# Kernel optimization log

Measured on AMD Instinct MI355X. Metric: run time of the kernel, lower is better.

## Reference

```python
import jax, jax.numpy as jnp
import numpy as np


def _cdist(A, B):
    # Euclidean distance matrix via the norm trick: ||a-b||^2 = |a|^2 + |b|^2 - 2 a.b
    # A: (M, D), B: (N, D) -> (M, N). Avoids materializing (M, N, D).
    a2 = jnp.sum(A * A, axis=-1)[:, None]
    b2 = jnp.sum(B * B, axis=-1)[None, :]
    d2 = a2 + b2 - 2.0 * (A @ B.T)
    return jnp.sqrt(jnp.maximum(d2, 0.0))


def _multiquadric(x):
    return jnp.sqrt(x * x + 1.0)


def setup_inputs() -> dict:
    key = jax.random.key(0)
    k1, k2, k3 = jax.random.split(key, 3)
    M, N, D, K = 16384, 8192, 3, 64
    Xp = jax.random.normal(k1, (M, D), dtype=jnp.float32)
    X = jax.random.normal(k2, (N, D), dtype=jnp.float32)
    W = jax.random.normal(k3, (K, N), dtype=jnp.float32)  # solved weights self.M: (K, N)
    eps = jnp.ones((), dtype=jnp.float32)
    return {"Xp": Xp, "X": X, "W": W, "eps": eps}


def reference(Xp, X, W, eps):
    # dist: (M, N) pairwise distances, phi = kernel(eps * dist)
    dist = _cdist(Xp, X)
    phi = _multiquadric(eps * dist)
    # Solve.forward: matmul(W, phi^T)^T == phi @ W^T -> (M, K)
    return phi @ W.T
```

## Files before the change

### kernel.cpp

```cpp
#include <hip/hip_runtime.h>
#include <hip/hip_bf16.h>
#include <stdint.h>

#define M_ROWS 16384
#define N_PTS  8192
#define K_OUT  64
#define NSPLIT 8
#define SLICE  (N_PTS / NSPLIT)

typedef short bf16x8 __attribute__((ext_vector_type(8)));
typedef float f32x4  __attribute__((ext_vector_type(4)));

union ABFrag { bf16x8 v; uint32_t u[4]; };
union BFrag  { uint4 q; bf16x8 v; };

__device__ __forceinline__ uint32_t pack_bf16_rhu(float a, float b) {
    uint32_t ua = __builtin_bit_cast(uint32_t, a) + 0x8000u;
    uint32_t ub = __builtin_bit_cast(uint32_t, b) + 0x8000u;
    return __builtin_amdgcn_perm(ub, ua, 0x07060302u);
}
__device__ __forceinline__ uint32_t pack_bf16_rne(float a, float b) {
    uint32_t ua = __builtin_bit_cast(uint32_t, a);
    ua += 0x7FFFu + ((ua >> 16) & 1u);
    uint32_t ub = __builtin_bit_cast(uint32_t, b);
    ub += 0x7FFFu + ((ub >> 16) & 1u);
    return __builtin_amdgcn_perm(ub, ua, 0x07060302u);
}

__global__ __launch_bounds__(256) void rbf_prep(
    const float* __restrict__ Wf, const float* __restrict__ X,
    const float* __restrict__ epsp, float* __restrict__ out,
    uint4* __restrict__ Wt, float* __restrict__ Xx,
    float* __restrict__ Xy, float* __restrict__ Xz)
{
    const int bid = blockIdx.x, tid = threadIdx.x;
    if (bid < 256) {
        const int kt = tid >> 6, lane = tid & 63;
        const int l15 = lane & 15, g = lane >> 4;
        const int row = kt * 16 + l15;
        const int col = bid * 32 + g * 8;
        const float4* src = (const float4*)(Wf + row * N_PTS + col);
        const float4 w0 = src[0], w1 = src[1];
        uint4 p;
        p.x = pack_bf16_rne(w0.x, w0.y);
        p.y = pack_bf16_rne(w0.z, w0.w);
        p.z = pack_bf16_rne(w1.x, w1.y);
        p.w = pack_bf16_rne(w1.z, w1.w);
        Wt[(bid * 4 + kt) * 64 + lane] = p;
    } else if (bid < 512) {
        const int i = ((bid - 256) * 256 + tid) * 4;
        const float4 z = make_float4(0.f, 0.f, 0.f, 0.f);
        float4* o = (float4*)out + i;
        o[0] = z; o[1] = z; o[2] = z; o[3] = z;
    } else {
        const int n = ((bid - 512) * 256 + tid) * 4;
        const float e = *epsp;
        const float4* p = (const float4*)(X + 3 * n);
        const float4 p0 = p[0], p1 = p[1], p2 = p[2];
        *(float4*)(Xx + n) = make_float4(p0.x * e, p0.w * e, p1.z * e, p2.y * e);
        *(float4*)(Xy + n) = make_float4(p0.y * e, p1.x * e, p1.w * e, p2.z * e);
        *(float4*)(Xz + n) = make_float4(p0.z * e, p1.y * e, p2.x * e, p2.w * e);
    }
}

__global__ __launch_bounds__(256, 4) void rbf_main(
    const float* __restrict__ Xp, const uint4* __restrict__ Wt,
    const float* __restrict__ Xx, const float* __restrict__ Xy,
    const float* __restrict__ Xz, const float* __restrict__ epsp,
    float* __restrict__ out)
{
    __shared__ float sX[SLICE], sY[SLICE], sZ[SLICE];

    const int tid  = threadIdx.x;
    const int lane = tid & 63;
    const int wv   = tid >> 6;
    const int l15  = lane & 15;
    const int g    = lane >> 4;

    const int bid  = blockIdx.x;
    const int ns   = bid & (NSPLIT - 1);
    const int rg   = bid >> 3;
    const int nbase = ns * SLICE;

    {
        const int i = tid * 4;
        *(float4*)(sX + i) = *(const float4*)(Xx + nbase + i);
        *(float4*)(sY + i) = *(const float4*)(Xy + nbase + i);
        *(float4*)(sZ + i) = *(const float4*)(Xz + nbase + i);
    }

    const float eps = *epsp;
    const int rowbase = rg * 128 + wv * 16;
    const int r0 = rowbase + l15;
    const int r1 = r0 + 64;
    const float px0 = Xp[r0 * 3 + 0] * eps, py0 = Xp[r0 * 3 + 1] * eps, pz0 = Xp[r0 * 3 + 2] * eps;
    const float px1 = Xp[r1 * 3 + 0] * eps, py1 = Xp[r1 * 3 + 1] * eps, pz1 = Xp[r1 * 3 + 2] * eps;

    __syncthreads();

    f32x4 acc00 = {0.f,0.f,0.f,0.f}, acc01 = acc00, acc02 = acc00, acc03 = acc00;
    f32x4 acc10 = acc00, acc11 = acc00, acc12 = acc00, acc13 = acc00;

    const uint4* wbase = Wt + (ns * 32) * 256 + lane;

    for (int s = 0; s < SLICE / 32; ++s) {
        const uint4* wp = wbase + s * 256;
        BFrag b0, b1, b2, b3;
        b0.q = wp[0];
        b1.q = wp[64];
        b2.q = wp[128];
        b3.q = wp[192];

        const int ci = s * 32 + g * 8;
        const float4 x0 = *(const float4*)(sX + ci), x1 = *(const float4*)(sX + ci + 4);
        const float4 y0 = *(const float4*)(sY + ci), y1 = *(const float4*)(sY + ci + 4);
        const float4 z0 = *(const float4*)(sZ + ci), z1 = *(const float4*)(sZ + ci + 4);

        const float xs[8] = {x0.x, x0.y, x0.z, x0.w, x1.x, x1.y, x1.z, x1.w};
        const float ys[8] = {y0.x, y0.y, y0.z, y0.w, y1.x, y1.y, y1.z, y1.w};
        const float zs[8] = {z0.x, z0.y, z0.z, z0.w, z1.x, z1.y, z1.z, z1.w};

        float t0[8], t1[8];
        #pragma unroll
        for (int j = 0; j < 8; ++j) {
            float dx = px0 - xs[j], dy = py0 - ys[j], dz = pz0 - zs[j];
            float d = fmaf(dx, dx, 1.0f); d = fmaf(dy, dy, d); d = fmaf(dz, dz, d);
            t0[j] = __builtin_amdgcn_sqrtf(d);
            dx = px1 - xs[j]; dy = py1 - ys[j]; dz = pz1 - zs[j];
            d = fmaf(dx, dx, 1.0f); d = fmaf(dy, dy, d); d = fmaf(dz, dz, d);
            t1[j] = __builtin_amdgcn_sqrtf(d);
        }

        ABFrag a0, a1;
        #pragma unroll
        for (int j = 0; j < 4; ++j) {
            a0.u[j] = pack_bf16_rhu(t0[2 * j], t0[2 * j + 1]);
            a1.u[j] = pack_bf16_rhu(t1[2 * j], t1[2 * j + 1]);
        }

        acc00 = __builtin_amdgcn_mfma_f32_16x16x32_bf16(a0.v, b0.v, acc00, 0, 0, 0);
        acc01 = __builtin_amdgcn_mfma_f32_16x16x32_bf16(a0.v, b1.v, acc01, 0, 0, 0);
        acc02 = __builtin_amdgcn_mfma_f32_16x16x32_bf16(a0.v, b2.v, acc02, 0, 0, 0);
        acc03 = __builtin_amdgcn_mfma_f32_16x16x32_bf16(a0.v, b3.v, acc03, 0, 0, 0);
        acc10 = __builtin_amdgcn_mfma_f32_16x16x32_bf16(a1.v, b0.v, acc10, 0, 0, 0);
        acc11 = __builtin_amdgcn_mfma_f32_16x16x32_bf16(a1.v, b1.v, acc11, 0, 0, 0);
        acc12 = __builtin_amdgcn_mfma_f32_16x16x32_bf16(a1.v, b2.v, acc12, 0, 0, 0);
        acc13 = __builtin_amdgcn_mfma_f32_16x16x32_bf16(a1.v, b3.v, acc13, 0, 0, 0);
    }

    float* o0 = out + (rowbase + g * 4) * K_OUT + l15;
    float* o1 = o0 + 64 * K_OUT;
    #pragma unroll
    for (int reg = 0; reg < 4; ++reg) {
        atomicAdd(o0 + reg * K_OUT +  0, acc00[reg]);
        atomicAdd(o0 + reg * K_OUT + 16, acc01[reg]);
        atomicAdd(o0 + reg * K_OUT + 32, acc02[reg]);
        atomicAdd(o0 + reg * K_OUT + 48, acc03[reg]);
        atomicAdd(o1 + reg * K_OUT +  0, acc10[reg]);
        atomicAdd(o1 + reg * K_OUT + 16, acc11[reg]);
        atomicAdd(o1 + reg * K_OUT + 32, acc12[reg]);
        atomicAdd(o1 + reg * K_OUT + 48, acc13[reg]);
    }
}

extern "C" void kernel_launch(void* const* d_in, const int* in_sizes, int n_in,
                              void* d_out, int out_size, void* d_ws, size_t ws_size,
                              hipStream_t stream) {
    (void)in_sizes; (void)n_in; (void)out_size; (void)ws_size;
    const float* Xp  = (const float*)d_in[0];
    const float* X   = (const float*)d_in[1];
    const float* Wf  = (const float*)d_in[2];
    const float* eps = (const float*)d_in[3];
    float* out = (float*)d_out;

    uint4* Wt = (uint4*)d_ws;
    float* Xx = (float*)((char*)d_ws + (1u << 20));
    float* Xy = Xx + N_PTS;
    float* Xz = Xy + N_PTS;

    rbf_prep<<<dim3(520), dim3(256), 0, stream>>>(Wf, X, eps, out, Wt, Xx, Xy, Xz);
    rbf_main<<<dim3((M_ROWS / 128) * NSPLIT), dim3(256), 0, stream>>>(Xp, Wt, Xx, Xy, Xz, eps, out);
}
```

Measured before the change: 111.3 us.

## Compute squared distances with MFMA via the norm trick, transpose phi through LDS

Replaces the per-element VALU distance computation with a bf16 MFMA that evaluates |p|^2 + |x|^2 + 1 - 2p·x from packed augmented vectors prepared in the prep kernel. The MFMA output layout is transposed through a small padded LDS tile to form the A operand of the phi·W^T MFMA. Rows per block are halved (grid doubled) and the occupancy hint is raised. The aim is to cut VALU work per phi element. The cost is bf16 precision on the coordinates and norms, which can cancel badly in the distance expansion, plus extra LDS traffic.

```diff
diff --git a/kernel.cpp b/kernel.cpp
--- a/kernel.cpp
+++ b/kernel.cpp
@@ -7,12 +7,12 @@
 #define K_OUT  64
 #define NSPLIT 8
 #define SLICE  (N_PTS / NSPLIT)
+#define LSTR   40
 
 typedef short bf16x8 __attribute__((ext_vector_type(8)));
 typedef float f32x4  __attribute__((ext_vector_type(4)));
 
-union ABFrag { bf16x8 v; uint32_t u[4]; };
-union BFrag  { uint4 q; bf16x8 v; };
+union ABFrag { bf16x8 v; uint32_t u[4]; uint4 q; };
 
 __device__ __forceinline__ uint32_t pack_bf16_rhu(float a, float b) {
     uint32_t ua = __builtin_bit_cast(uint32_t, a) + 0x8000u;
@@ -30,8 +30,7 @@
 __global__ __launch_bounds__(256) void rbf_prep(
     const float* __restrict__ Wf, const float* __restrict__ X,
     const float* __restrict__ epsp, float* __restrict__ out,
-    uint4* __restrict__ Wt, float* __restrict__ Xx,
-    float* __restrict__ Xy, float* __restrict__ Xz)
+    uint4* __restrict__ Wt, uint4* __restrict__ Pf)
 {
     const int bid = blockIdx.x, tid = threadIdx.x;
     if (bid < 256) {
@@ -53,113 +52,117 @@
         float4* o = (float4*)out + i;
         o[0] = z; o[1] = z; o[2] = z; o[3] = z;
     } else {
-        const int n = ((bid - 512) * 256 + tid) * 4;
-        const float e = *epsp;
-        const float4* p = (const float4*)(X + 3 * n);
-        const float4 p0 = p[0], p1 = p[1], p2 = p[2];
-        *(float4*)(Xx + n) = make_float4(p0.x * e, p0.w * e, p1.z * e, p2.y * e);
-        *(float4*)(Xy + n) = make_float4(p0.y * e, p1.x * e, p1.w * e, p2.z * e);
-        *(float4*)(Xz + n) = make_float4(p0.z * e, p1.y * e, p2.x * e, p2.w * e);
+        const int idx = (bid - 512) * 256 + tid;
+        const int lane = idx & 63;
+        const int t = idx >> 6;
+        const int g = lane >> 4, i = lane & 15;
+        uint4 v = make_uint4(0u, 0u, 0u, 0u);
+        if (g == 0) {
+            const int pt = t * 16 + i;
+            const float e = *epsp;
+            const float x = X[3 * pt + 0] * e;
+            const float y = X[3 * pt + 1] * e;
+            const float z = X[3 * pt + 2] * e;
+            const float b = fmaf(x, x, fmaf(y, y, fmaf(z, z, 1.0f)));
+            v.x = pack_bf16_rne(x, y);
+            v.y = pack_bf16_rne(z, b);
+            v.z = pack_bf16_rne(1.0f, 0.0f);
+        }
+        Pf[idx] = v;
     }
 }
 
-__global__ __launch_bounds__(256, 4) void rbf_main(
+__global__ __launch_bounds__(256, 5) void rbf_main(
     const float* __restrict__ Xp, const uint4* __restrict__ Wt,
-    const float* __restrict__ Xx, const float* __restrict__ Xy,
-    const float* __restrict__ Xz, const float* __restrict__ epsp,
+    const uint4* __restrict__ Pf, const float* __restrict__ epsp,
     float* __restrict__ out)
 {
-    __shared__ float sX[SLICE], sY[SLICE], sZ[SLICE];
+    __shared__ __align__(16) short sPhi[4 * 16 * LSTR];
 
     const int tid  = threadIdx.x;
     const int lane = tid & 63;
     const int wv   = tid >> 6;
-    const int l15  = lane & 15;
+    const int m    = lane & 15;
     const int g    = lane >> 4;
 
-    const int bid  = blockIdx.x;
-    const int ns   = bid & (NSPLIT - 1);
-    const int rg   = bid >> 3;
+    const int bid   = blockIdx.x;
+    const int ns    = bid & (NSPLIT - 1);
+    const int rg    = bid >> 3;
     const int nbase = ns * SLICE;
+    const int rowbase = rg * 64 + wv * 16;
 
-    {
-        const int i = tid * 4;
-        *(float4*)(sX + i) = *(const float4*)(Xx + nbase + i);
-        *(float4*)(sY + i) = *(const float4*)(Xy + nbase + i);
-        *(float4*)(sZ + i) = *(const float4*)(Xz + nbase + i);
+    ABFrag b1;
+    b1.q = make_uint4(0u, 0u, 0u, 0u);
+    if (g == 0) {
+        const float e = *epsp;
+        const int r = rowbase + m;
+        const float px = Xp[3 * r + 0] * e;
+        const float py = Xp[3 * r + 1] * e;
+        const float pz = Xp[3 * r + 2] * e;
+        const float a = fmaf(px, px, fmaf(py, py, pz * pz));
+        b1.u[0] = pack_bf16_rne(-2.0f * px, -2.0f * py);
+        b1.u[1] = pack_bf16_rne(-2.0f * pz, 1.0f);
+        b1.u[2] = pack_bf16_rne(a, 0.0f);
     }
 
-    const float eps = *epsp;
-    const int rowbase = rg * 128 + wv * 16;
-    const int r0 = rowbase + l15;
-    const int r1 = r0 + 64;
-    const float px0 = Xp[r0 * 3 + 0] * eps, py0 = Xp[r0 * 3 + 1] * eps, pz0 = Xp[r0 * 3 + 2] * eps;
-    const float px1 = Xp[r1 * 3 + 0] * eps, py1 = Xp[r1 * 3 + 1] * eps, pz1 = Xp[r1 * 3 + 2] * eps;
+    f32x4 acc0 = {0.f, 0.f, 0.f, 0.f};
+    f32x4 acc1 = acc0, acc2 = acc0, acc3 = acc0;
 
-    __syncthreads();
+    const uint4* pA = Pf + (nbase >> 4) * 64 + lane;
+    const uint4* wb = Wt + ns * 32 * 256 + lane;
+    short* wrow = sPhi + (wv * 16 + m) * LSTR;
 
-    f32x4 acc00 = {0.f,0.f,0.f,0.f}, acc01 = acc00, acc02 = acc00, acc03 = acc00;
-    f32x4 acc10 = acc00, acc11 = acc00, acc12 = acc00, acc13 = acc00;
+    #pragma unroll 2
+    for (int s = 0; s < SLICE / 32; ++s) {
+        ABFrag a1a, a1b;
+        a1a.q = pA[s * 128];
+        a1b.q = pA[s * 128 + 64];
 
-    const uint4* wbase = Wt + (ns * 32) * 256 + lane;
+        const uint4* wp = wb + s * 256;
+        ABFrag w0, w1, w2, w3;
+        w0.q = wp[0];
+        w1.q = wp[64];
+        w2.q = wp[128];
+        w3.q = wp[192];
 
-    for (int s = 0; s < SLICE / 32; ++s) {
-        const uint4* wp = wbase + s * 256;
-        BFrag b0, b1, b2, b3;
-        b0.q = wp[0];
-        b1.q = wp[64];
-        b2.q = wp[128];
-        b3.q = wp[192];
+        const f32x4 zc = {0.f, 0.f, 0.f, 0.f};
+        f32x4 d1a = __builtin_amdgcn_mfma_f32_16x16x32_bf16(a1a.v, b1.v, zc, 0, 0, 0);
+        f32x4 d1b = __builtin_amdgcn_mfma_f32_16x16x32_bf16(a1b.v, b1.v, zc, 0, 0, 0);
 
-        const int ci = s * 32 + g * 8;
-        const float4 x0 = *(const float4*)(sX + ci), x1 = *(const float4*)(sX + ci + 4);
-        const float4 y0 = *(const float4*)(sY + ci), y1 = *(const float4*)(sY + ci + 4);
-        const float4 z0 = *(const float4*)(sZ + ci), z1 = *(const float4*)(sZ + ci + 4);
+        float t0 = __builtin_amdgcn_sqrtf(fmaxf(d1a[0], 0.f));
+        float t1 = __builtin_amdgcn_sqrtf(fmaxf(d1a[1], 0.f));
+        float t2 = __builtin_amdgcn_sqrtf(fmaxf(d1a[2], 0.f));
+        float t3 = __builtin_amdgcn_sqrtf(fmaxf(d1a[3], 0.f));
+        float t4 = __builtin_amdgcn_sqrtf(fmaxf(d1b[0], 0.f));
+        float t5 = __builtin_amdgcn_sqrtf(fmaxf(d1b[1], 0.f));
+        float t6 = __builtin_amdgcn_sqrtf(fmaxf(d1b[2], 0.f));
+        float t7 = __builtin_amdgcn_sqrtf(fmaxf(d1b[3], 0.f));
 
-        const float xs[8] = {x0.x, x0.y, x0.z, x0.w, x1.x, x1.y, x1.z, x1.w};
-        const float ys[8] = {y0.x, y0.y, y0.z, y0.w, y1.x, y1.y, y1.z, y1.w};
-        const float zs[8] = {z0.x, z0.y, z0.z, z0.w, z1.x, z1.y, z1.z, z1.w};
+        uint2 pa, pb;
+        pa.x = pack_bf16_rhu(t0, t1);
+        pa.y = pack_bf16_rhu(t2, t3);
+        pb.x = pack_bf16_rhu(t4, t5);
+        pb.y = pack_bf16_rhu(t6, t7);
 
-        float t0[8], t1[8];
-        #pragma unroll
-        for (int j = 0; j < 8; ++j) {
-            float dx = px0 - xs[j], dy = py0 - ys[j], dz = pz0 - zs[j];
-            float d = fmaf(dx, dx, 1.0f); d = fmaf(dy, dy, d); d = fmaf(dz, dz, d);
-            t0[j] = __builtin_amdgcn_sqrtf(d);
-            dx = px1 - xs[j]; dy = py1 - ys[j]; dz = pz1 - zs[j];
-            d = fmaf(dx, dx, 1.0f); d = fmaf(dy, dy, d); d = fmaf(dz, dz, d);
-            t1[j] = __builtin_amdgcn_sqrtf(d);
-        }
+        *(uint2*)(wrow + 4 * g)      = pa;
+        *(uint2*)(wrow + 16 + 4 * g) = pb;
 
-        ABFrag a0, a1;
-        #pragma unroll
-        for (int j = 0; j < 4; ++j) {
-            a0.u[j] = pack_bf16_rhu(t0[2 * j], t0[2 * j + 1]);
-            a1.u[j] = pack_bf16_rhu(t1[2 * j], t1[2 * j + 1]);
-        }
+        ABFrag a2;
+        a2.q = *(const uint4*)(wrow + 8 * g);
 
-        acc00 = __builtin_amdgcn_mfma_f32_16x16x32_bf16(a0.v, b0.v, acc00, 0, 0, 0);
-        acc01 = __builtin_amdgcn_mfma_f32_16x16x32_bf16(a0.v, b1.v, acc01, 0, 0, 0);
-        acc02 = __builtin_amdgcn_mfma_f32_16x16x32_bf16(a0.v, b2.v, acc02, 0, 0, 0);
-        acc03 = __builtin_amdgcn_mfma_f32_16x16x32_bf16(a0.v, b3.v, acc03, 0, 0, 0);
-        acc10 = __builtin_amdgcn_mfma_f32_16x16x32_bf16(a1.v, b0.v, acc10, 0, 0, 0);
-        acc11 = __builtin_amdgcn_mfma_f32_16x16x32_bf16(a1.v, b1.v, acc11, 0, 0, 0);
-        acc12 = __builtin_amdgcn_mfma_f32_16x16x32_bf16(a1.v, b2.v, acc12, 0, 0, 0);
-        acc13 = __builtin_amdgcn_mfma_f32_16x16x32_bf16(a1.v, b3.v, acc13, 0, 0, 0);
+        acc0 = __builtin_amdgcn_mfma_f32_16x16x32_bf16(a2.v, w0.v, acc0, 0, 0, 0);
+        acc1 = __builtin_amdgcn_mfma_f32_16x16x32_bf16(a2.v, w1.v, acc1, 0, 0, 0);
+        acc2 = __builtin_amdgcn_mfma_f32_16x16x32_bf16(a2.v, w2.v, acc2, 0, 0, 0);
+        acc3 = __builtin_amdgcn_mfma_f32_16x16x32_bf16(a2.v, w3.v, acc3, 0, 0, 0);
     }
 
-    float* o0 = out + (rowbase + g * 4) * K_OUT + l15;
-    float* o1 = o0 + 64 * K_OUT;
+    float* o = out + (rowbase + g * 4) * K_OUT + m;
     #pragma unroll
     for (int reg = 0; reg < 4; ++reg) {
-        atomicAdd(o0 + reg * K_OUT +  0, acc00[reg]);
-        atomicAdd(o0 + reg * K_OUT + 16, acc01[reg]);
-        atomicAdd(o0 + reg * K_OUT + 32, acc02[reg]);
-        atomicAdd(o0 + reg * K_OUT + 48, acc03[reg]);
-        atomicAdd(o1 + reg * K_OUT +  0, acc10[reg]);
-        atomicAdd(o1 + reg * K_OUT + 16, acc11[reg]);
-        atomicAdd(o1 + reg * K_OUT + 32, acc12[reg]);
-        atomicAdd(o1 + reg * K_OUT + 48, acc13[reg]);
+        atomicAdd(o + reg * K_OUT +  0, acc0[reg]);
+        atomicAdd(o + reg * K_OUT + 16, acc1[reg]);
+        atomicAdd(o + reg * K_OUT + 32, acc2[reg]);
+        atomicAdd(o + reg * K_OUT + 48, acc3[reg]);
     }
 }
 
@@ -174,10 +177,8 @@
     float* out = (float*)d_out;
 
     uint4* Wt = (uint4*)d_ws;
-    float* Xx = (float*)((char*)d_ws + (1u << 20));
-    float* Xy = Xx + N_PTS;
-    float* Xz = Xy + N_PTS;
+    uint4* Pf = (uint4*)((char*)d_ws + (1u << 20));
 
-    rbf_prep<<<dim3(520), dim3(256), 0, stream>>>(Wf, X, eps, out, Wt, Xx, Xy, Xz);
-    rbf_main<<<dim3((M_ROWS / 128) * NSPLIT), dim3(256), 0, stream>>>(Xp, Wt, Xx, Xy, Xz, eps, out);
+    rbf_prep<<<dim3(640), dim3(256), 0, stream>>>(Wf, X, eps, out, Wt, Pf);
+    rbf_main<<<dim3((M_ROWS / 64) * NSPLIT), dim3(256), 0, stream>>>(Xp, Wt, Pf, eps, out);
 }
```

Result: slower. 120.5 us (+8.3%).
